# Kernel optimization log

Hardware: AMD Instinct MI355X
Metric: run time of the kernel (lower is better)

Reference implementation:

```python
import jax, jax.numpy as jnp
import numpy as np

N = 200000
E = 6400000
NEG_SLOPE = 0.01  # nn.LeakyReLU default

def _leaky(x):
    return jnp.where(x >= 0, x, NEG_SLOPE * x)

def gcn_conv(x, edge_index, W, b, n):
    # PyG GCNConv: add self-loops, symmetric degree norm, linear, scatter-add, bias
    src, dst = edge_index[0], edge_index[1]
    loops = jnp.arange(n, dtype=src.dtype)
    src = jnp.concatenate([src, loops])
    dst = jnp.concatenate([dst, loops])
    deg = jax.ops.segment_sum(jnp.ones_like(dst, dtype=x.dtype), dst, num_segments=n)
    dinv = jnp.where(deg > 0, jax.lax.rsqrt(deg), 0.0)
    norm = dinv[src] * dinv[dst]                  # [E+N]
    h = x @ W.T                                   # [N,50] linear (no bias yet)
    msg = h[src] * norm[:, None]                  # gather + scale
    out = jax.ops.segment_sum(msg, dst, num_segments=n)  # scatter-add to targets
    return out + b

def setup_inputs() -> dict:
    key = jax.random.key(0)
    ks = jax.random.split(key, 20)
    def w(k, o, i):
        return jax.random.normal(k, (o, i), dtype=jnp.float32) * (1.0 / np.sqrt(i))
    def bvec(k, o):
        return jax.random.normal(k, (o,), dtype=jnp.float32) * 0.01
    inp = {
        'x': jax.random.normal(ks[0], (N, 150), dtype=jnp.float32),
        'edge_index': jax.random.randint(ks[1], (2, E), 0, N, dtype=jnp.int64 if jax.config.jax_enable_x64 else jnp.int32),
        'epsilon': jax.random.normal(ks[2], (N, 10), dtype=jnp.float32),
        'Wg': w(ks[3], 50, 50), 'bg': bvec(ks[4], 50),
        'We1': w(ks[5], 40, 50), 'be1': bvec(ks[6], 40),
        'We2': w(ks[7], 30, 40), 'be2': bvec(ks[8], 30),
        'We3': w(ks[9], 20, 30), 'be3': bvec(ks[10], 20),
        'Wfc': w(ks[11], 10, 10), 'bfc': bvec(ks[12], 10),
        'Wd1': w(ks[13], 20, 10), 'bd1': bvec(ks[14], 20),
        'Wd2': w(ks[15], 40, 20), 'bd2': bvec(ks[16], 40),
        'Wd3': w(ks[17], 50, 40), 'bd3': bvec(ks[18], 50),
    }
    return inp

def reference(x, edge_index, epsilon, Wg, bg, We1, be1, We2, be2, We3, be3,
              Wfc, bfc, Wd1, bd1, Wd2, bd2, Wd3, bd3):
    x1 = x[:, 100:]                                   # [N,50]
    h = gcn_conv(x1, edge_index, Wg, bg, x.shape[0])  # [N,50]
    # encoder
    e = _leaky(h @ We1.T + be1)
    e = _leaky(e @ We2.T + be2)
    e = e @ We3.T + be3                               # [N,20]
    mu, log_var = e[:, :10], e[:, 10:]
    # reparameterization: mu + eps * sqrt(exp(log_var))
    z1 = mu + epsilon * jnp.exp(0.5 * log_var)
    z = jax.nn.relu(z1 @ Wfc.T + bfc)                 # FC
    # decoder
    d = _leaky(z @ Wd1.T + bd1)
    d = _leaky(d @ Wd2.T + bd2)
    mu_prime = jax.nn.sigmoid(d @ Wd3.T + bd3)        # [N,50]
    return (mu_prime, mu, log_var, z)
```

## Files before the change

kernel.cpp:

```cpp
#include <hip/hip_runtime.h>


#define NEG 0.01f
#define GS 64
#define ELLS 64
#define SLICES 16
#define SPILL_CAP 65536

static __device__ __forceinline__ float bf2f(unsigned short u) {
    return __uint_as_float(((unsigned)u) << 16);
}
static __device__ __forceinline__ float leaky(float a) { return (a >= 0.f) ? a : NEG * a; }

__global__ void k_zero(int* __restrict__ indeg, int* __restrict__ flag, int n) {
    int i = blockIdx.x * 256 + threadIdx.x;
    if (i < n) indeg[i] = 0;
    if (i == 0) { flag[0] = 0; flag[1] = 0; flag[2] = 0; }
}

__global__ void k_detect(const unsigned* __restrict__ x, long xwords,
                         const unsigned* __restrict__ ei, long epairs,
                         int* __restrict__ flag) {
    const long stride = 2048L * 256;
    if (blockIdx.x < 2048) {
        long i = (long)blockIdx.x * 256 + threadIdx.x;
        int c = 0;
        for (; i < xwords; i += stride) {
            unsigned w = x[i];
            if (((w >> 23) & 0xFFu) == 0xFFu || ((w >> 7) & 0xFFu) == 0xFFu) c++;
        }
        if (c) atomicAdd(&flag[0], c);
    } else {
        long i = (long)(blockIdx.x - 2048) * 256 + threadIdx.x;
        int c = 0;
        for (; i < epairs; i += stride)
            if (ei[2 * i + 1] == 0u) c++;
        if (c) atomicAdd(&flag[1], c);
    }
}

__global__ void k_build(const int* __restrict__ ei, int* __restrict__ indeg,
                        int* __restrict__ ebuf, int2* __restrict__ spill,
                        int* __restrict__ flag, int E, int N) {
    int blk = blockIdx.x;
    int pass = blk >> 12;
    int x = blk & 7;
    int q = (blk & 4095) >> 3;
    int s = pass * 8 + x;
    int sw = (N + SLICES - 1) / SLICES;
    int nlo = s * sw;
    int nhi = nlo + sw; if (nhi > N) nhi = N;
    bool is64 = flag[1] > (E >> 1);
    for (long e = (long)q * 256 + threadIdx.x; e < E; e += 512L * 256) {
        int d = is64 ? ei[2 * (E + e)] : ei[E + e];
        if (d < nlo || d >= nhi) continue;
        int src = is64 ? ei[2 * e] : ei[e];
        if ((unsigned)src >= (unsigned)N) continue;
        int c = atomicAdd(&indeg[d], 1);
        if (c < ELLS) {
            ebuf[(size_t)d * ELLS + c] = src;
        } else {
            int o = atomicAdd(&flag[2], 1);
            if (o < SPILL_CAP) spill[o] = make_int2(src, d);
        }
    }
}

__global__ void k_dinv(const int* __restrict__ indeg, float* __restrict__ dinv, int n) {
    int i = blockIdx.x * 256 + threadIdx.x;
    if (i < n) dinv[i] = rsqrtf(1.0f + (float)indeg[i]);
}

struct CW {
    const void* src[16];
    int off[16];
    int n[16];
};
__global__ void k_convw(CW cw, float* __restrict__ dst, const int* __restrict__ flag) {
    int b = blockIdx.x;
    bool isf = flag[0] > 64;
    const float* sf = (const float*)cw.src[b];
    const unsigned short* sh = (const unsigned short*)cw.src[b];
    float* d = dst + cw.off[b];
    int n = cw.n[b];
    for (int i = threadIdx.x; i < n; i += 256) d[i] = isf ? sf[i] : bf2f(sh[i]);
}

#define O_WG 0
#define O_BG 2500
#define O_WE1 2550
#define O_BE1 4550
#define O_WE2 4590
#define O_BE2 5790
#define O_WE3 5820
#define O_BE3 6420
#define O_WFC 6440
#define O_BFC 6540
#define O_WD1 6550
#define O_BD1 6750
#define O_WD2 6770
#define O_BD2 7570
#define O_WD3 7610
#define O_BD3 9610
#define W_TOT 9660

__global__ __launch_bounds__(256) void k_g(const void* __restrict__ xv,
                                           const float* __restrict__ W,
                                           const float* __restrict__ dinv,
                                           const int* __restrict__ flag,
                                           float* __restrict__ g, int n) {
    int i = blockIdx.x * 256 + threadIdx.x;
    if (i >= n) return;
    bool isf = flag[0] > 64;
    float xr[50];
    if (isf) {
        const float* p = (const float*)xv + (size_t)i * 150 + 100;
#pragma unroll
        for (int k = 0; k < 50; k++) xr[k] = p[k];
    } else {
        const unsigned short* p = (const unsigned short*)xv + (size_t)i * 150 + 100;
#pragma unroll
        for (int k = 0; k < 50; k++) xr[k] = bf2f(p[k]);
    }
    const float* Wg = W + O_WG;
    float di = dinv[i];
    float* gr = g + (size_t)i * GS;
#pragma unroll
    for (int f = 0; f < 50; f += 2) {
        float a0 = 0.f, a1 = 0.f;
#pragma unroll
        for (int p = 0; p < 50; p++) {
            a0 += Wg[f * 50 + p] * xr[p];
            a1 += Wg[(f + 1) * 50 + p] * xr[p];
        }
        gr[f] = a0 * di;
        gr[f + 1] = a1 * di;
    }
}

__global__ __launch_bounds__(256) void k_gather(const float* __restrict__ g,
                                                const int* __restrict__ indeg,
                                                const int* __restrict__ ebuf,
                                                const float* __restrict__ dinv,
                                                const float* __restrict__ W,
                                                float* __restrict__ h1, int n) {
    int wid = threadIdx.x >> 6;
    int lane = threadIdx.x & 63;
    int i = blockIdx.x * 4 + wid;
    if (i >= n) return;
    int fc = lane < 50 ? lane : 49;
    int cnt = indeg[i];
    if (cnt > ELLS) cnt = ELLS;
    float di = dinv[i];
    int ev = (lane < cnt) ? ebuf[(size_t)i * ELLS + lane] : 0;
    float a0 = g[(size_t)i * GS + fc];
    float a1 = 0.f, a2 = 0.f, a3 = 0.f, a4 = 0.f, a5 = 0.f, a6 = 0.f, a7 = 0.f;
    int m = 0;
    for (; m + 7 < cnt; m += 8) {
        int j0 = __shfl(ev, m);
        int j1 = __shfl(ev, m + 1);
        int j2 = __shfl(ev, m + 2);
        int j3 = __shfl(ev, m + 3);
        int j4 = __shfl(ev, m + 4);
        int j5 = __shfl(ev, m + 5);
        int j6 = __shfl(ev, m + 6);
        int j7 = __shfl(ev, m + 7);
        a0 += g[(size_t)j0 * GS + fc];
        a1 += g[(size_t)j1 * GS + fc];
        a2 += g[(size_t)j2 * GS + fc];
        a3 += g[(size_t)j3 * GS + fc];
        a4 += g[(size_t)j4 * GS + fc];
        a5 += g[(size_t)j5 * GS + fc];
        a6 += g[(size_t)j6 * GS + fc];
        a7 += g[(size_t)j7 * GS + fc];
    }
    for (; m < cnt; m++) {
        int j = __shfl(ev, m);
        a0 += g[(size_t)j * GS + fc];
    }
    if (lane < 50) {
        float h = (((a0 + a1) + (a2 + a3)) + ((a4 + a5) + (a6 + a7))) * di + W[O_BG + lane];
        h1[(size_t)i * 50 + lane] = h;
    }
}

__global__ void k_spill(const int2* __restrict__ spill, const int* __restrict__ flag,
                        const float* __restrict__ g, const float* __restrict__ dinv,
                        float* __restrict__ h1) {
    int nov = flag[2];
    if (nov > SPILL_CAP) nov = SPILL_CAP;
    int lane = threadIdx.x & 63;
    int wave = (blockIdx.x * 256 + threadIdx.x) >> 6;
    for (int e = wave; e < nov; e += gridDim.x * 4) {
        int2 sd = spill[e];
        if (lane < 50)
            atomicAdd(&h1[(size_t)sd.y * 50 + lane], g[(size_t)sd.x * GS + lane] * dinv[sd.y]);
    }
}


__global__ __launch_bounds__(256) void k_e1(const float* __restrict__ h1,
                                            const float* __restrict__ W,
                                            float* __restrict__ t1, int n) {
    int i = blockIdx.x * 256 + threadIdx.x;
    if (i >= n) return;
    float v0[50];
    const float2* hr = (const float2*)(h1 + (size_t)i * 50);
#pragma unroll
    for (int p = 0; p < 25; p++) {
        float2 q = hr[p];
        v0[2 * p] = q.x;
        v0[2 * p + 1] = q.y;
    }
    float o[40];
#pragma unroll
    for (int f = 0; f < 40; f++) {
        float a = W[O_BE1 + f];
#pragma unroll
        for (int p = 0; p < 50; p++) a += W[O_WE1 + f * 50 + p] * v0[p];
        o[f] = leaky(a);
    }
    float4* ot = (float4*)(t1 + (size_t)i * 40);
#pragma unroll
    for (int p = 0; p < 10; p++) ot[p] = make_float4(o[4 * p], o[4 * p + 1], o[4 * p + 2], o[4 * p + 3]);
}

__global__ __launch_bounds__(256) void k_e23(const float* __restrict__ t1,
                                             const float* __restrict__ W,
                                             float* __restrict__ out, int n) {
    int i = blockIdx.x * 256 + threadIdx.x;
    if (i >= n) return;
    float v1[40];
    const float4* tr = (const float4*)(t1 + (size_t)i * 40);
#pragma unroll
    for (int p = 0; p < 10; p++) {
        float4 q = tr[p];
        v1[4 * p] = q.x; v1[4 * p + 1] = q.y; v1[4 * p + 2] = q.z; v1[4 * p + 3] = q.w;
    }
    float v2[30];
#pragma unroll
    for (int f = 0; f < 30; f++) {
        float a = W[O_BE2 + f];
#pragma unroll
        for (int p = 0; p < 40; p++) a += W[O_WE2 + f * 40 + p] * v1[p];
        v2[f] = leaky(a);
    }
    float v3[20];
#pragma unroll
    for (int f = 0; f < 20; f++) {
        float a = W[O_BE3 + f];
#pragma unroll
        for (int p = 0; p < 30; p++) a += W[O_WE3 + f * 30 + p] * v2[p];
        v3[f] = a;
    }
    float2* o_mu = (float2*)(out + (size_t)n * 50 + (size_t)i * 10);
    float2* o_lv = (float2*)(out + (size_t)n * 60 + (size_t)i * 10);
#pragma unroll
    for (int p = 0; p < 5; p++) {
        o_mu[p] = make_float2(v3[2 * p], v3[2 * p + 1]);
        o_lv[p] = make_float2(v3[10 + 2 * p], v3[10 + 2 * p + 1]);
    }
}

__global__ __launch_bounds__(256) void k_zfc(float* outb,
                                             const void* __restrict__ epsv,
                                             const float* __restrict__ W,
                                             const int* __restrict__ flag,
                                             float* __restrict__ t3, int n) {
    int i = blockIdx.x * 256 + threadIdx.x;
    if (i >= n) return;
    bool isf = flag[0] > 64;
    float mu[10], lv[10];
    const float2* pm = (const float2*)(outb + (size_t)n * 50 + (size_t)i * 10);
    const float2* pl = (const float2*)(outb + (size_t)n * 60 + (size_t)i * 10);
#pragma unroll
    for (int p = 0; p < 5; p++) {
        float2 a = pm[p]; mu[2 * p] = a.x; mu[2 * p + 1] = a.y;
        float2 b = pl[p]; lv[2 * p] = b.x; lv[2 * p + 1] = b.y;
    }
    float ev[10];
    if (isf) {
        const float* p = (const float*)epsv + (size_t)i * 10;
#pragma unroll
        for (int k = 0; k < 10; k++) ev[k] = p[k];
    } else {
        const unsigned short* p = (const unsigned short*)epsv + (size_t)i * 10;
#pragma unroll
        for (int k = 0; k < 10; k++) ev[k] = bf2f(p[k]);
    }
    float z1[10];
#pragma unroll
    for (int k = 0; k < 10; k++) z1[k] = mu[k] + ev[k] * expf(0.5f * lv[k]);
    float z[10];
#pragma unroll
    for (int f = 0; f < 10; f++) {
        float a = W[O_BFC + f];
#pragma unroll
        for (int p = 0; p < 10; p++) a += W[O_WFC + f * 10 + p] * z1[p];
        z[f] = (a > 0.f) ? a : 0.f;
    }
    float2* o_z = (float2*)(outb + (size_t)n * 70 + (size_t)i * 10);
#pragma unroll
    for (int p = 0; p < 5; p++) o_z[p] = make_float2(z[2 * p], z[2 * p + 1]);
    float d1[20];
#pragma unroll
    for (int f = 0; f < 20; f++) {
        float a = W[O_BD1 + f];
#pragma unroll
        for (int p = 0; p < 10; p++) a += W[O_WD1 + f * 10 + p] * z[p];
        d1[f] = leaky(a);
    }
    float d2[40];
#pragma unroll
    for (int f = 0; f < 40; f++) {
        float a = W[O_BD2 + f];
#pragma unroll
        for (int p = 0; p < 20; p++) a += W[O_WD2 + f * 20 + p] * d1[p];
        d2[f] = leaky(a);
    }
    float4* ot = (float4*)(t3 + (size_t)i * 40);
#pragma unroll
    for (int p = 0; p < 10; p++)
        ot[p] = make_float4(d2[4 * p], d2[4 * p + 1], d2[4 * p + 2], d2[4 * p + 3]);
}

__global__ __launch_bounds__(256) void k_d3(const float* __restrict__ t3,
                                            const float* __restrict__ W,
                                            float* __restrict__ out, int n) {
    int i = blockIdx.x * 256 + threadIdx.x;
    if (i >= n) return;
    float d2[40];
    const float4* tr = (const float4*)(t3 + (size_t)i * 40);
#pragma unroll
    for (int p = 0; p < 10; p++) {
        float4 q = tr[p];
        d2[4 * p] = q.x; d2[4 * p + 1] = q.y; d2[4 * p + 2] = q.z; d2[4 * p + 3] = q.w;
    }
    float o[50];
#pragma unroll
    for (int f = 0; f < 50; f++) {
        float a = W[O_BD3 + f];
#pragma unroll
        for (int p = 0; p < 40; p++) a += W[O_WD3 + f * 40 + p] * d2[p];
        o[f] = 1.f / (1.f + expf(-a));
    }
    float2* om = (float2*)(out + (size_t)i * 50);
#pragma unroll
    for (int p = 0; p < 25; p++) om[p] = make_float2(o[2 * p], o[2 * p + 1]);
}

extern "C" void kernel_launch(void* const* d_in, const int* in_sizes, int n_in,
                              void* d_out, int out_size, void* d_ws, size_t ws_size,
                              hipStream_t stream) {
    const int N = in_sizes[0] / 150;
    const int E = in_sizes[1] / 2;

    char* w = (char*)d_ws;
    auto alloc = [&](size_t bytes) {
        void* p = (void*)w;
        w += (bytes + 255) & ~(size_t)255;
        return p;
    };
    int* indeg = (int*)alloc((size_t)N * 4);
    int* flag = (int*)alloc(256);
    float* dinv = (float*)alloc((size_t)N * 4);
    float* Wall = (float*)alloc((size_t)W_TOT * 4);
    int2* spill = (int2*)alloc((size_t)SPILL_CAP * 8);
    float* g = (float*)alloc((size_t)N * GS * 4);
    float* h1 = (float*)alloc((size_t)N * 50 * 4);
    int* ebuf = (int*)alloc((size_t)N * ELLS * 4);

    float* t1 = g;
    float* t3 = h1;

    CW cw;
    static const int wn[16] = {2500, 50, 2000, 40, 1200, 30, 600, 20,
                               100, 10, 200, 20, 800, 40, 2000, 50};
    static const int wo[16] = {O_WG, O_BG, O_WE1, O_BE1, O_WE2, O_BE2, O_WE3, O_BE3,
                               O_WFC, O_BFC, O_WD1, O_BD1, O_WD2, O_BD2, O_WD3, O_BD3};
    for (int k = 0; k < 16; k++) {
        cw.src[k] = d_in[3 + k];
        cw.off[k] = wo[k];
        cw.n[k] = wn[k];
    }

    int nbN = (N + 255) / 256;

    k_zero<<<nbN, 256, 0, stream>>>(indeg, flag, N);
    k_detect<<<4096, 256, 0, stream>>>((const unsigned*)d_in[0], (long)N * 75,
                                       (const unsigned*)d_in[1], (long)E, flag);
    k_build<<<8192, 256, 0, stream>>>((const int*)d_in[1], indeg, ebuf, spill, flag, E, N);
    k_dinv<<<nbN, 256, 0, stream>>>(indeg, dinv, N);
    k_convw<<<16, 256, 0, stream>>>(cw, Wall, flag);
    k_g<<<nbN, 256, 0, stream>>>(d_in[0], Wall, dinv, flag, g, N);
    k_gather<<<(N + 3) / 4, 256, 0, stream>>>(g, indeg, ebuf, dinv, Wall, h1, N);
    k_spill<<<64, 256, 0, stream>>>(spill, flag, g, dinv, h1);
    k_e1<<<nbN, 256, 0, stream>>>(h1, Wall, t1, N);
    k_e23<<<nbN, 256, 0, stream>>>(t1, Wall, (float*)d_out, N);
    k_zfc<<<nbN, 256, 0, stream>>>((float*)d_out, d_in[2], Wall, flag, t3, N);
    k_d3<<<nbN, 256, 0, stream>>>(t3, Wall, (float*)d_out, N);
}
```

Baseline: 1.054 ms.

## Sample dtype detection and compact edge indices to int32 before ELL build

The format-detection kernel now inspects only a sampled subset of the input (1024 chunks of 1024 words per side) instead of scanning all of x and edge_index. A new compaction kernel converts edge_index once into dense int32 src/dst arrays, placed in the scratch g buffer when it fits. The 16-slice build kernel then reads these with 4-wide nontemporal vector loads instead of re-reading strided 64-bit indices on every slice pass. Sampling makes detection heuristic and could misjudge unusual inputs. Compaction also adds one extra read/write pass over the edges.

```diff
diff --git a/kernel.cpp b/kernel.cpp
--- a/kernel.cpp
+++ b/kernel.cpp
@@ -7,6 +7,11 @@
 #define SLICES 16
 #define SPILL_CAP 65536
 
+#define DET_ES (1024 * 1024)
+#define IS64_THRESH (DET_ES / 2)
+
+typedef int vint4 __attribute__((ext_vector_type(4)));
+
 static __device__ __forceinline__ float bf2f(unsigned short u) {
     return __uint_as_float(((unsigned)u) << 16);
 }
@@ -21,47 +26,93 @@
 __global__ void k_detect(const unsigned* __restrict__ x, long xwords,
                          const unsigned* __restrict__ ei, long epairs,
                          int* __restrict__ flag) {
+    int gw = (blockIdx.x * 256 + threadIdx.x) >> 6;
+    int lane = threadIdx.x & 63;
+    int side = gw >> 10;
+    int ch = gw & 1023;
+    int c = 0;
+    if (side == 0) {
+        long step = xwords >> 10;
+        long base = (long)ch * step;
+        if (base + 1024 > xwords) base = xwords > 1024 ? xwords - 1024 : 0;
+#pragma unroll
+        for (int t = 0; t < 16; t++) {
+            long idx = base + t * 64 + lane;
+            if (idx < xwords) {
+                unsigned w = x[idx];
+                if (((w >> 23) & 0xFFu) == 0xFFu || ((w >> 7) & 0xFFu) == 0xFFu) c++;
+            }
+        }
+        for (int k = 32; k; k >>= 1) c += __shfl_xor(c, k);
+        if (lane == 0 && c) atomicAdd(&flag[0], c);
+    } else {
+        long step = epairs >> 10;
+        long base = (long)ch * step;
+        if (base + 1024 > epairs) base = epairs > 1024 ? epairs - 1024 : 0;
+#pragma unroll
+        for (int t = 0; t < 16; t++) {
+            long idx = base + t * 64 + lane;
+            if (idx < epairs && ei[2 * idx + 1] == 0u) c++;
+        }
+        for (int k = 32; k; k >>= 1) c += __shfl_xor(c, k);
+        if (lane == 0 && c) atomicAdd(&flag[1], c);
+    }
+}
+
+__global__ void k_compact(const unsigned* __restrict__ ei, const int* __restrict__ flag,
+                          int* __restrict__ src32, int* __restrict__ dst32, long E) {
+    bool is64 = flag[1] > IS64_THRESH;
+    long i = (long)blockIdx.x * 256 + threadIdx.x;
     const long stride = 2048L * 256;
-    if (blockIdx.x < 2048) {
-        long i = (long)blockIdx.x * 256 + threadIdx.x;
-        int c = 0;
-        for (; i < xwords; i += stride) {
-            unsigned w = x[i];
-            if (((w >> 23) & 0xFFu) == 0xFFu || ((w >> 7) & 0xFFu) == 0xFFu) c++;
-        }
-        if (c) atomicAdd(&flag[0], c);
+    if (is64) {
+        const int2* p = (const int2*)ei;
+        for (; i < E; i += stride) {
+            src32[i] = p[i].x;
+            dst32[i] = p[E + i].x;
+        }
     } else {
-        long i = (long)(blockIdx.x - 2048) * 256 + threadIdx.x;
-        int c = 0;
-        for (; i < epairs; i += stride)
-            if (ei[2 * i + 1] == 0u) c++;
-        if (c) atomicAdd(&flag[1], c);
-    }
-}
-
-__global__ void k_build(const int* __restrict__ ei, int* __restrict__ indeg,
+        const int* p = (const int*)ei;
+        for (; i < E; i += stride) {
+            src32[i] = p[i];
+            dst32[i] = p[E + i];
+        }
+    }
+}
+
+__global__ __launch_bounds__(256) void k_build(const int* __restrict__ src32,
+                        const int* __restrict__ dst32, int* __restrict__ indeg,
                         int* __restrict__ ebuf, int2* __restrict__ spill,
                         int* __restrict__ flag, int E, int N) {
     int blk = blockIdx.x;
     int pass = blk >> 12;
-    int x = blk & 7;
+    int xg = blk & 7;
     int q = (blk & 4095) >> 3;
-    int s = pass * 8 + x;
+    int s = pass * 8 + xg;
     int sw = (N + SLICES - 1) / SLICES;
     int nlo = s * sw;
     int nhi = nlo + sw; if (nhi > N) nhi = N;
-    bool is64 = flag[1] > (E >> 1);
-    for (long e = (long)q * 256 + threadIdx.x; e < E; e += 512L * 256) {
-        int d = is64 ? ei[2 * (E + e)] : ei[E + e];
-        if (d < nlo || d >= nhi) continue;
-        int src = is64 ? ei[2 * e] : ei[e];
-        if ((unsigned)src >= (unsigned)N) continue;
-        int c = atomicAdd(&indeg[d], 1);
-        if (c < ELLS) {
-            ebuf[(size_t)d * ELLS + c] = src;
+    const long step = 512L * 256 * 4;
+    for (long e0 = ((long)q * 256 + threadIdx.x) * 4; e0 < E; e0 += step) {
+        int dv[4];
+        if (e0 + 4 <= E) {
+            vint4 t = __builtin_nontemporal_load((const vint4*)(dst32 + e0));
+            dv[0] = t.x; dv[1] = t.y; dv[2] = t.z; dv[3] = t.w;
         } else {
-            int o = atomicAdd(&flag[2], 1);
-            if (o < SPILL_CAP) spill[o] = make_int2(src, d);
+            for (int k = 0; k < 4; k++) dv[k] = (e0 + k < E) ? dst32[e0 + k] : -1;
+        }
+#pragma unroll
+        for (int k = 0; k < 4; k++) {
+            int d = dv[k];
+            if (d < nlo || d >= nhi) continue;
+            int src = __builtin_nontemporal_load(&src32[e0 + k]);
+            if ((unsigned)src >= (unsigned)N) continue;
+            int c = atomicAdd(&indeg[d], 1);
+            if (c < ELLS) {
+                ebuf[(size_t)d * ELLS + c] = src;
+            } else {
+                int o = atomicAdd(&flag[2], 1);
+                if (o < SPILL_CAP) spill[o] = make_int2(src, d);
+            }
         }
     }
 }
@@ -370,6 +421,16 @@
     float* h1 = (float*)alloc((size_t)N * 50 * 4);
     int* ebuf = (int*)alloc((size_t)N * ELLS * 4);
 
+    int* dst32;
+    int* src32;
+    if (2L * E <= (long)N * GS) {
+        dst32 = (int*)g;
+        src32 = (int*)g + E;
+    } else {
+        dst32 = (int*)alloc((size_t)E * 4);
+        src32 = (int*)alloc((size_t)E * 4);
+    }
+
     float* t1 = g;
     float* t3 = h1;
 
@@ -387,9 +448,10 @@
     int nbN = (N + 255) / 256;
 
     k_zero<<<nbN, 256, 0, stream>>>(indeg, flag, N);
-    k_detect<<<4096, 256, 0, stream>>>((const unsigned*)d_in[0], (long)N * 75,
-                                       (const unsigned*)d_in[1], (long)E, flag);
-    k_build<<<8192, 256, 0, stream>>>((const int*)d_in[1], indeg, ebuf, spill, flag, E, N);
+    k_detect<<<512, 256, 0, stream>>>((const unsigned*)d_in[0], (long)N * 75,
+                                      (const unsigned*)d_in[1], (long)E, flag);
+    k_compact<<<2048, 256, 0, stream>>>((const unsigned*)d_in[1], flag, src32, dst32, (long)E);
+    k_build<<<8192, 256, 0, stream>>>(src32, dst32, indeg, ebuf, spill, flag, E, N);
     k_dinv<<<nbN, 256, 0, stream>>>(indeg, dinv, N);
     k_convw<<<16, 256, 0, stream>>>(cw, Wall, flag);
     k_g<<<nbN, 256, 0, stream>>>(d_in[0], Wall, dinv, flag, g, N);
```

Result: faster. 1.028 ms (-2.5%).
